# Kernel tuning notes

Measured on AMD Instinct MI355X. Metric: run time of the kernel, lower is better.

## Reference

```python
import jax, jax.numpy as jnp
import numpy as np

VOCAB, S, E, H = 50000, 64, 256, 256
T, B = 512, 64


def _lstm_dir(x_seq, h0, c0, Wih, Whh, bih, bhh):
    """Single-direction LSTM. x_seq: [T,B,E] -> [T,B,H]. PyTorch gate order i,f,g,o."""
    def step(carry, x):
        h, c = carry
        gates = x @ Wih.T + h @ Whh.T + (bih + bhh)  # [B,4H]
        i, f, g, o = jnp.split(gates, 4, axis=-1)
        c = jax.nn.sigmoid(f) * c + jax.nn.sigmoid(i) * jnp.tanh(g)
        h = jax.nn.sigmoid(o) * jnp.tanh(c)
        return (h, c), h
    (_, _), hs = jax.lax.scan(step, (h0, c0), x_seq)
    return hs


def setup_inputs() -> dict:
    key = jax.random.key(0)
    ks = jax.random.split(key, 16)
    k = 1.0 / np.sqrt(H)
    u = lambda kk, shp: jax.random.uniform(kk, shp, jnp.float32, -k, k)
    inp = {
        "obs_seq": jax.random.randint(ks[0], (T, B), 0, VOCAB),
        "h0": jax.random.normal(ks[1], (2, B, H), jnp.float32),
        "c0": jax.random.normal(ks[2], (2, B, H), jnp.float32),
        "embed_table": jax.random.normal(ks[3], (VOCAB, E), jnp.float32),
        "Wih_f": u(ks[4], (4 * H, E)), "Whh_f": u(ks[5], (4 * H, H)),
        "bih_f": u(ks[6], (4 * H,)), "bhh_f": u(ks[7], (4 * H,)),
        "Wih_b": u(ks[8], (4 * H, E)), "Whh_b": u(ks[9], (4 * H, H)),
        "bih_b": u(ks[10], (4 * H,)), "bhh_b": u(ks[11], (4 * H,)),
        "W_lin": u(ks[12], (S, 2 * H)), "b_lin": u(ks[13], (S,)),
        "pairwise": jax.random.normal(ks[14], (S, S), jnp.float32),
        "start": jax.random.normal(jax.random.fold_in(key, 7), (S,), jnp.float32),
        "stop": jax.random.normal(ks[15], (S,), jnp.float32),
    }
    return inp


def reference(obs_seq, h0, c0, embed_table, Wih_f, Whh_f, bih_f, bhh_f,
              Wih_b, Whh_b, bih_b, bhh_b, W_lin, b_lin, pairwise, start, stop):
    # BiLSTM features
    emb = embed_table[obs_seq]  # [T,B,E]
    hs_f = _lstm_dir(emb, h0[0], c0[0], Wih_f, Whh_f, bih_f, bhh_f)
    hs_b = _lstm_dir(emb[::-1], h0[1], c0[1], Wih_b, Whh_b, bih_b, bhh_b)[::-1]
    feats = jnp.concatenate([hs_f, hs_b], axis=-1)  # [T,B,2H]
    # Emission scores
    scores = jnp.einsum('tbf,sf->tbs', feats, W_lin) + b_lin  # [T,B,S]
    # Viterbi DP (max-plus over states)
    delta0 = start[None, :] + scores[0]  # [B,S]

    def vstep(delta, s_t):
        m = delta[:, :, None] + pairwise[None, :, :]  # [B, prev, next]
        bp = jnp.argmax(m, axis=1)                    # [B,S]
        return jnp.max(m, axis=1) + s_t, bp

    delta_T, bps = jax.lax.scan(vstep, delta0, scores[1:])  # bps: [T-1,B,S]
    final = delta_T + stop[None, :]
    max_score = jnp.max(final, axis=-1)          # [B]
    last = jnp.argmax(final, axis=-1)            # [B]

    def bstep(state, bp_t):
        prev = jnp.take_along_axis(bp_t, state[:, None], axis=1)[:, 0]
        return prev, state

    state0, states_rest = jax.lax.scan(bstep, last, bps, reverse=True)
    state_seq = jnp.concatenate([state0[None], states_rest], axis=0)  # [T,B]
    return max_score, state_seq
```

## Files before the change

### kernel.cpp

```cpp
#include <hip/hip_runtime.h>
#include <math.h>

constexpr int TT = 512;
constexpr int BB = 64;
constexpr int EE = 256;
constexpr int HH = 256;
constexpr int SS = 64;
constexpr int BH = BB * HH;
constexpr int SLICE = 2048;
constexpr int DIRSZ = TT * 8 * SLICE;

typedef float v2f __attribute__((ext_vector_type(2)));

__global__ __launch_bounds__(256) void embT_prep(
    const int* __restrict__ obs, const float* __restrict__ embed,
    float* __restrict__ embT2)
{
    const int t   = blockIdx.x;
    const int tid = threadIdx.x;
    const int b   = tid & 63;
    const int kc  = tid >> 6;
    const int tok = obs[t * BB + b];
    const float4* er = (const float4*)(embed + (size_t)tok * EE);
    float* dst = embT2 + ((size_t)t * 8 + (b >> 3)) * SLICE + (b & 7);
    #pragma unroll
    for (int i = 0; i < 16; ++i) {
        const int k4 = kc * 16 + i;
        float4 v = er[k4];
        const int k = k4 * 4;
        dst[(k + 0) * 8] = v.x;
        dst[(k + 1) * 8] = v.y;
        dst[(k + 2) * 8] = v.z;
        dst[(k + 3) * 8] = v.w;
    }
}

__global__ __launch_bounds__(256) void weight_prep(
    const float* __restrict__ Wih_f, const float* __restrict__ Whh_f,
    const float* __restrict__ Wih_b, const float* __restrict__ Whh_b,
    float* __restrict__ WBx, float* __restrict__ WBh)
{
    const int bx  = blockIdx.x;
    const int dir = bx & 1;
    const int ug  = (bx >> 1) & 15;
    const int kc  = bx >> 5;
    const int tid = threadIdx.x;
    const float* Wih = dir ? Wih_b : Wih_f;
    const float* Whh = dir ? Whh_b : Whh_f;
    const size_t base = (((size_t)(dir * 16 + ug) * 8 + kc) * 32) * 64;
    #pragma unroll
    for (int i = 0; i < 8; ++i) {
        const int idx = tid + i * 256;
        const int kl  = idx >> 6;
        const int r   = idx & 63;
        const int row = (r >> 4) * 256 + ug * 16 + (r & 15);
        const int k   = kc * 32 + kl;
        WBx[base + (size_t)kl * 64 + r] = Wih[(size_t)row * EE + k];
        WBh[base + (size_t)kl * 64 + r] = Whh[(size_t)row * HH + k];
    }
}

__global__ __launch_bounds__(512) void lstm_grid(
    const float* __restrict__ embT2,
    const float* __restrict__ WBx, const float* __restrict__ WBh,
    const float* __restrict__ bih_f, const float* __restrict__ bhh_f,
    const float* __restrict__ bih_b, const float* __restrict__ bhh_b,
    const float* __restrict__ h0, const float* __restrict__ c0,
    float* __restrict__ HS2f, float* __restrict__ HS2b)
{
    __shared__ __align__(16) float xbuf[2][SLICE];
    __shared__ __align__(16) float hbuf[SLICE];
    __shared__ float pb[8 * 520];

    const int tid = threadIdx.x;
    const int r   = tid & 63;
    const int kc  = tid >> 6;
    const int bx  = blockIdx.x;
    const int dir = bx & 1;
    const int ug  = (bx >> 1) & 15;
    const int sg  = bx >> 5;
    const int u0  = ug * 16;

    const float* bih = dir ? bih_b : bih_f;
    const float* bhh = dir ? bhh_b : bhh_f;
    float* HS = dir ? HS2b : HS2f;

    const size_t wbase = (((size_t)(dir * 16 + ug) * 8 + kc) * 32) * 64 + r;
    const float* wx = WBx + wbase;
    const float* wh = WBh + wbase;

    const int uL = tid >> 3;
    const int sU = tid & 7;
    float c_reg = 0.0f;
    float bias0 = 0.f, bias1 = 0.f, bias2 = 0.f, bias3 = 0.f;
    if (tid < 128) {
        const int u  = u0 + uL;
        const int bg = sg * 8 + sU;
        c_reg = c0[dir * BH + bg * HH + u];
        bias0 = bih[0 * 256 + u] + bhh[0 * 256 + u];
        bias1 = bih[1 * 256 + u] + bhh[1 * 256 + u];
        bias2 = bih[2 * 256 + u] + bhh[2 * 256 + u];
        bias3 = bih[3 * 256 + u] + bhh[3 * 256 + u];
    }

    {
        const int t0 = dir ? (TT - 1) : 0;
        const float4 xv = *(const float4*)(embT2
            + ((size_t)t0 * 8 + sg) * SLICE + (size_t)tid * 4);
        *(float4*)&xbuf[0][tid * 4] = xv;
        #pragma unroll
        for (int j = 0; j < 4; ++j) {
            const int idx = tid * 4 + j;
            const int u = idx >> 3, s = idx & 7;
            hbuf[idx] = h0[dir * BH + (sg * 8 + s) * HH + u];
        }
    }
    __syncthreads();

    for (int step = 0; step < TT; ++step) {
        const int t   = dir ? (TT - 1 - step) : step;
        const int cur = step & 1;

        v2f A0 = {0.f, 0.f}, A1 = {0.f, 0.f}, A2 = {0.f, 0.f}, A3 = {0.f, 0.f};

        {
            const float4* xb4 = (const float4*)&xbuf[cur][kc * 256];
            #pragma unroll 8
            for (int kl = 0; kl < 32; ++kl) {
                const float wv = wx[kl * 64];
                const v2f w2 = {wv, wv};
                const float4 xa = xb4[kl * 2];
                const float4 xc = xb4[kl * 2 + 1];
                A0 = __builtin_elementwise_fma((v2f){xa.x, xa.y}, w2, A0);
                A1 = __builtin_elementwise_fma((v2f){xa.z, xa.w}, w2, A1);
                A2 = __builtin_elementwise_fma((v2f){xc.x, xc.y}, w2, A2);
                A3 = __builtin_elementwise_fma((v2f){xc.z, xc.w}, w2, A3);
            }
        }

        const bool has_next = (step + 1 < TT);
        float4 xnext;
        if (has_next) {
            const int tn = dir ? (TT - 2 - step) : (step + 1);
            xnext = *(const float4*)(embT2
                + ((size_t)tn * 8 + sg) * SLICE + (size_t)tid * 4);
        }

        if (step > 0) {
            const int tp = dir ? (t + 1) : (t - 1);
            const float* hsrc = HS + ((size_t)tp * 8 + sg) * SLICE
                                + kc * 256 + r;
            float h0v, h1v, h2v, h3v;
            int spins = 0;
            for (;;) {
                asm volatile(
                    "global_load_dword %0, %4, off sc0 sc1\n\t"
                    "global_load_dword %1, %4, off offset:256 sc0 sc1\n\t"
                    "global_load_dword %2, %4, off offset:512 sc0 sc1\n\t"
                    "global_load_dword %3, %4, off offset:768 sc0 sc1\n\t"
                    "s_waitcnt vmcnt(0)"
                    : "=v"(h0v), "=v"(h1v), "=v"(h2v), "=v"(h3v)
                    : "v"(hsrc)
                    : "memory");
                const float ssum = (h0v + h1v) + (h2v + h3v);
                if (!__any(ssum != ssum)) break;
                if (++spins > 200000) break;
            }
            const int hb = kc * 256 + r;
            hbuf[hb      ] = h0v;
            hbuf[hb +  64] = h1v;
            hbuf[hb + 128] = h2v;
            hbuf[hb + 192] = h3v;
        }

        if (has_next) *(float4*)&xbuf[cur ^ 1][tid * 4] = xnext;

        {
            const float4* hb4 = (const float4*)&hbuf[kc * 256];
            #pragma unroll 8
            for (int kl = 0; kl < 32; ++kl) {
                const float wv = wh[kl * 64];
                const v2f w2 = {wv, wv};
                const float4 ha = hb4[kl * 2];
                const float4 hc = hb4[kl * 2 + 1];
                A0 = __builtin_elementwise_fma((v2f){ha.x, ha.y}, w2, A0);
                A1 = __builtin_elementwise_fma((v2f){ha.z, ha.w}, w2, A1);
                A2 = __builtin_elementwise_fma((v2f){hc.x, hc.y}, w2, A2);
                A3 = __builtin_elementwise_fma((v2f){hc.z, hc.w}, w2, A3);
            }
        }

        {
            const int pbi = kc * 64 + r;
            pb[0 * 520 + pbi] = A0.x; pb[1 * 520 + pbi] = A0.y;
            pb[2 * 520 + pbi] = A1.x; pb[3 * 520 + pbi] = A1.y;
            pb[4 * 520 + pbi] = A2.x; pb[5 * 520 + pbi] = A2.y;
            pb[6 * 520 + pbi] = A3.x; pb[7 * 520 + pbi] = A3.y;
        }
        __syncthreads();

        if (tid < 128) {
            float p0 = bias0, p1 = bias1, p2 = bias2, p3 = bias3;
            #pragma unroll
            for (int q = 0; q < 8; ++q) {
                p0 += pb[sU * 520 + q * 64 + 0 * 16 + uL];
                p1 += pb[sU * 520 + q * 64 + 1 * 16 + uL];
                p2 += pb[sU * 520 + q * 64 + 2 * 16 + uL];
                p3 += pb[sU * 520 + q * 64 + 3 * 16 + uL];
            }
            const float ig = 1.0f / (1.0f + expf(-p0));
            const float fg = 1.0f / (1.0f + expf(-p1));
            const float gg = tanhf(p2);
            const float og = 1.0f / (1.0f + expf(-p3));
            c_reg = fg * c_reg + ig * gg;
            const float h = og * tanhf(c_reg);
            unsigned* dst = (unsigned*)(HS + ((size_t)t * 8 + sg) * SLICE
                                        + (u0 + uL) * 8 + sU);
            (void)__hip_atomic_exchange(dst, __float_as_uint(h),
                                        __ATOMIC_RELAXED,
                                        __HIP_MEMORY_SCOPE_AGENT);
        }
    }
}

__global__ __launch_bounds__(256) void scores_kernel(
    const float* __restrict__ HS2f, const float* __restrict__ HS2b,
    const float* __restrict__ W_lin, const float* __restrict__ b_lin,
    float* __restrict__ scores)
{
    __shared__ __align__(16) float As[128 * 64];
    __shared__ __align__(16) float Ws[128 * 64];
    const int t   = blockIdx.x;
    const int tid = threadIdx.x;
    const int bl  = tid & 63;
    const int kc  = tid >> 6;
    const int tb  = tid & 15;
    const int ts  = tid >> 4;

    float acc[4][4] = {};

    for (int chunk = 0; chunk < 4; ++chunk) {
        const int koff = chunk * 128;
        const float* srcH = (koff < 256) ? HS2f : HS2b;
        const int bu = koff & 255;
        #pragma unroll
        for (int i = 0; i < 8; ++i) {
            const int jg = tid + i * 256;
            const int sg = jg >> 8;
            const int j  = jg & 255;
            const int kl = j >> 1;
            const int s0 = (j & 1) * 4;
            const float4 v = *(const float4*)(srcH
                + ((size_t)t * 8 + sg) * SLICE + (size_t)(bu + kl) * 8 + s0);
            *(float4*)&As[kl * 64 + sg * 8 + s0] = v;
        }
        const float4* wl4 = (const float4*)(W_lin + koff);
        #pragma unroll
        for (int it = 0; it < 8; ++it) {
            const int k4 = it * 4 + kc;
            float4 wv = wl4[bl * 128 + k4];
            const int k = k4 * 4;
            Ws[(k + 0) * 64 + bl] = wv.x; Ws[(k + 1) * 64 + bl] = wv.y;
            Ws[(k + 2) * 64 + bl] = wv.z; Ws[(k + 3) * 64 + bl] = wv.w;
        }
        __syncthreads();
        #pragma unroll 4
        for (int k = 0; k < 128; ++k) {
            const float4 av = *(const float4*)&As[k * 64 + tb * 4];
            const float4 bv = *(const float4*)&Ws[k * 64 + ts * 4];
            acc[0][0] += av.x * bv.x; acc[0][1] += av.x * bv.y; acc[0][2] += av.x * bv.z; acc[0][3] += av.x * bv.w;
            acc[1][0] += av.y * bv.x; acc[1][1] += av.y * bv.y; acc[1][2] += av.y * bv.z; acc[1][3] += av.y * bv.w;
            acc[2][0] += av.z * bv.x; acc[2][1] += av.z * bv.y; acc[2][2] += av.z * bv.z; acc[2][3] += av.z * bv.w;
            acc[3][0] += av.w * bv.x; acc[3][1] += av.w * bv.y; acc[3][2] += av.w * bv.z; acc[3][3] += av.w * bv.w;
        }
        __syncthreads();
    }

    #pragma unroll
    for (int i = 0; i < 4; ++i) {
        const int bb = tb * 4 + i;
        #pragma unroll
        for (int j = 0; j < 4; ++j) {
            const int ss = ts * 4 + j;
            scores[(size_t)t * (BB * SS) + bb * SS + ss] = acc[i][j] + b_lin[ss];
        }
    }
}

__global__ __launch_bounds__(256) void viterbi_kernel(
    const float* __restrict__ scores, const float* __restrict__ pairwise,
    const float* __restrict__ start, const float* __restrict__ stop,
    float* __restrict__ out)
{
    __shared__ float delta[2][64];
    __shared__ float part[4][64];
    __shared__ int   pidx[4][64];
    __shared__ unsigned char bps[511 * 64];
    __shared__ float fin[64];

    const int b   = blockIdx.x;
    const int tid = threadIdx.x;
    const int s   = tid & 63;
    const int q   = tid >> 6;

    float pw[16];
    #pragma unroll
    for (int i = 0; i < 16; ++i)
        pw[i] = pairwise[(q * 16 + i) * 64 + s];

    if (q == 0) delta[0][s] = start[s] + scores[b * SS + s];
    __syncthreads();

    int cur = 0;
    for (int t = 1; t < TT; ++t) {
        float sc = 0.0f;
        if (q == 0) sc = scores[(size_t)t * (BB * SS) + b * SS + s];
        float best = -1e30f;
        int bp = q * 16;
        #pragma unroll
        for (int i = 0; i < 16; ++i) {
            const float v = delta[cur][q * 16 + i] + pw[i];
            if (v > best) { best = v; bp = q * 16 + i; }
        }
        part[q][s] = best;
        pidx[q][s] = bp;
        __syncthreads();
        if (q == 0) {
            float m = part[0][s];
            int arg = pidx[0][s];
            #pragma unroll
            for (int qq = 1; qq < 4; ++qq) {
                const float v = part[qq][s];
                if (v > m) { m = v; arg = pidx[qq][s]; }
            }
            delta[cur ^ 1][s] = m + sc;
            bps[(t - 1) * 64 + s] = (unsigned char)arg;
        }
        cur ^= 1;
        __syncthreads();
    }

    if (q == 0) fin[s] = delta[cur][s] + stop[s];
    __syncthreads();

    if (tid == 0) {
        float m = fin[0];
        int arg = 0;
        for (int p = 1; p < 64; ++p)
            if (fin[p] > m) { m = fin[p]; arg = p; }
        out[b] = m;
        int st = arg;
        out[64 + 511 * 64 + b] = (float)st;
        for (int k = 510; k >= 0; --k) {
            st = bps[k * 64 + st];
            out[64 + k * 64 + b] = (float)st;
        }
    }
}

extern "C" void kernel_launch(void* const* d_in, const int* in_sizes, int n_in,
                              void* d_out, int out_size, void* d_ws, size_t ws_size,
                              hipStream_t stream)
{
    const int*   obs      = (const int*)d_in[0];
    const float* h0       = (const float*)d_in[1];
    const float* c0       = (const float*)d_in[2];
    const float* embed    = (const float*)d_in[3];
    const float* Wih_f    = (const float*)d_in[4];
    const float* Whh_f    = (const float*)d_in[5];
    const float* bih_f    = (const float*)d_in[6];
    const float* bhh_f    = (const float*)d_in[7];
    const float* Wih_b    = (const float*)d_in[8];
    const float* Whh_b    = (const float*)d_in[9];
    const float* bih_b    = (const float*)d_in[10];
    const float* bhh_b    = (const float*)d_in[11];
    const float* W_lin    = (const float*)d_in[12];
    const float* b_lin    = (const float*)d_in[13];
    const float* pairwise = (const float*)d_in[14];
    const float* start    = (const float*)d_in[15];
    const float* stop     = (const float*)d_in[16];
    (void)in_sizes; (void)n_in; (void)out_size; (void)ws_size;

    float* ws     = (float*)d_ws;
    float* embT2  = ws;
    float* HS2f   = embT2 + (size_t)DIRSZ;
    float* HS2b   = HS2f + (size_t)DIRSZ;
    float* scores = HS2b + (size_t)DIRSZ;
    float* WBx = scores;
    float* WBh = scores + (size_t)2 * 16 * 8 * 32 * 64;

    hipMemsetAsync(HS2f, 0xFF, (size_t)2 * DIRSZ * sizeof(float), stream);
    embT_prep<<<512, 256, 0, stream>>>(obs, embed, embT2);
    weight_prep<<<256, 256, 0, stream>>>(Wih_f, Whh_f, Wih_b, Whh_b, WBx, WBh);
    lstm_grid<<<256, 512, 0, stream>>>(
        embT2, WBx, WBh, bih_f, bhh_f, bih_b, bhh_b, h0, c0, HS2f, HS2b);
    scores_kernel<<<512, 256, 0, stream>>>(HS2f, HS2b, W_lin, b_lin, scores);
    viterbi_kernel<<<64, 256, 0, stream>>>(scores, pairwise, start, stop, (float*)d_out);
}
```

Before: 2.005 ms.

## Double hidden units per LSTM block, halving persistent grid to 128 blocks

```diff
diff --git a/kernel.cpp b/kernel.cpp
--- a/kernel.cpp
+++ b/kernel.cpp
@@ -42,25 +42,25 @@
 {
     const int bx  = blockIdx.x;
     const int dir = bx & 1;
-    const int ug  = (bx >> 1) & 15;
-    const int kc  = bx >> 5;
+    const int j   = (bx >> 1) & 7;
+    const int kc  = bx >> 4;
     const int tid = threadIdx.x;
     const float* Wih = dir ? Wih_b : Wih_f;
     const float* Whh = dir ? Whh_b : Whh_f;
-    const size_t base = (((size_t)(dir * 16 + ug) * 8 + kc) * 32) * 64;
+    const size_t base = (((size_t)(dir * 8 + j) * 8 + kc) * 32) * 128;
     #pragma unroll
-    for (int i = 0; i < 8; ++i) {
+    for (int i = 0; i < 16; ++i) {
         const int idx = tid + i * 256;
-        const int kl  = idx >> 6;
-        const int r   = idx & 63;
-        const int row = (r >> 4) * 256 + ug * 16 + (r & 15);
+        const int kl  = idx >> 7;
+        const int rg  = idx & 127;
+        const int row = (rg >> 5) * 256 + j * 32 + (rg & 31);
         const int k   = kc * 32 + kl;
-        WBx[base + (size_t)kl * 64 + r] = Wih[(size_t)row * EE + k];
-        WBh[base + (size_t)kl * 64 + r] = Whh[(size_t)row * HH + k];
-    }
-}
-
-__global__ __launch_bounds__(512) void lstm_grid(
+        WBx[base + (size_t)kl * 128 + rg] = Wih[(size_t)row * EE + k];
+        WBh[base + (size_t)kl * 128 + rg] = Whh[(size_t)row * HH + k];
+    }
+}
+
+__global__ __launch_bounds__(1024) void lstm_grid(
     const float* __restrict__ embT2,
     const float* __restrict__ WBx, const float* __restrict__ WBh,
     const float* __restrict__ bih_f, const float* __restrict__ bhh_f,
@@ -69,23 +69,27 @@
     float* __restrict__ HS2f, float* __restrict__ HS2b)
 {
     __shared__ __align__(16) float xbuf[2][SLICE];
-    __shared__ __align__(16) float hbuf[SLICE];
-    __shared__ float pb[8 * 520];
-
-    const int tid = threadIdx.x;
-    const int r   = tid & 63;
-    const int kc  = tid >> 6;
-    const int bx  = blockIdx.x;
-    const int dir = bx & 1;
-    const int ug  = (bx >> 1) & 15;
-    const int sg  = bx >> 5;
-    const int u0  = ug * 16;
+    __shared__ __align__(16) float hbuf[2][SLICE];
+    __shared__ float pb[8 * 1032];
+
+    const int tid  = threadIdx.x;
+    const int r    = tid & 63;
+    const int w    = tid >> 6;
+    const int kc   = w >> 1;
+    const int half = w & 1;
+    const int rg   = half * 64 + r;
+    const int bx   = blockIdx.x;
+    const int g    = bx & 15;
+    const int j    = bx >> 4;
+    const int dir  = g & 1;
+    const int sg   = g >> 1;
+    const int u0   = j * 32;
 
     const float* bih = dir ? bih_b : bih_f;
     const float* bhh = dir ? bhh_b : bhh_f;
     float* HS = dir ? HS2b : HS2f;
 
-    const size_t wbase = (((size_t)(dir * 16 + ug) * 8 + kc) * 32) * 64 + r;
+    const size_t wbase = (((size_t)(dir * 8 + j) * 8 + kc) * 32) * 128 + rg;
     const float* wx = WBx + wbase;
     const float* wh = WBh + wbase;
 
@@ -93,7 +97,7 @@
     const int sU = tid & 7;
     float c_reg = 0.0f;
     float bias0 = 0.f, bias1 = 0.f, bias2 = 0.f, bias3 = 0.f;
-    if (tid < 128) {
+    if (tid < 256) {
         const int u  = u0 + uL;
         const int bg = sg * 8 + sU;
         c_reg = c0[dir * BH + bg * HH + u];
@@ -105,14 +109,16 @@
 
     {
         const int t0 = dir ? (TT - 1) : 0;
-        const float4 xv = *(const float4*)(embT2
-            + ((size_t)t0 * 8 + sg) * SLICE + (size_t)tid * 4);
-        *(float4*)&xbuf[0][tid * 4] = xv;
+        const float2 xv = *(const float2*)(embT2
+            + ((size_t)t0 * 8 + sg) * SLICE + (size_t)tid * 2);
+        *(float2*)&xbuf[0][tid * 2] = xv;
         #pragma unroll
-        for (int j = 0; j < 4; ++j) {
-            const int idx = tid * 4 + j;
+        for (int jj = 0; jj < 2; ++jj) {
+            const int idx = tid * 2 + jj;
             const int u = idx >> 3, s = idx & 7;
-            hbuf[idx] = h0[dir * BH + (sg * 8 + s) * HH + u];
+            const float v = h0[dir * BH + (sg * 8 + s) * HH + u];
+            hbuf[0][idx] = v;
+            hbuf[1][idx] = v;
         }
     }
     __syncthreads();
@@ -127,7 +133,7 @@
             const float4* xb4 = (const float4*)&xbuf[cur][kc * 256];
             #pragma unroll 8
             for (int kl = 0; kl < 32; ++kl) {
-                const float wv = wx[kl * 64];
+                const float wv = wx[kl * 128];
                 const v2f w2 = {wv, wv};
                 const float4 xa = xb4[kl * 2];
                 const float4 xc = xb4[kl * 2 + 1];
@@ -139,11 +145,11 @@
         }
 
         const bool has_next = (step + 1 < TT);
-        float4 xnext;
+        float2 xnext;
         if (has_next) {
             const int tn = dir ? (TT - 2 - step) : (step + 1);
-            xnext = *(const float4*)(embT2
-                + ((size_t)tn * 8 + sg) * SLICE + (size_t)tid * 4);
+            xnext = *(const float2*)(embT2
+                + ((size_t)tn * 8 + sg) * SLICE + (size_t)tid * 2);
         }
 
         if (step > 0) {
@@ -167,19 +173,19 @@
                 if (++spins > 200000) break;
             }
             const int hb = kc * 256 + r;
-            hbuf[hb      ] = h0v;
-            hbuf[hb +  64] = h1v;
-            hbuf[hb + 128] = h2v;
-            hbuf[hb + 192] = h3v;
-        }
-
-        if (has_next) *(float4*)&xbuf[cur ^ 1][tid * 4] = xnext;
+            hbuf[half][hb      ] = h0v;
+            hbuf[half][hb +  64] = h1v;
+            hbuf[half][hb + 128] = h2v;
+            hbuf[half][hb + 192] = h3v;
+        }
+
+        if (has_next) *(float2*)&xbuf[cur ^ 1][tid * 2] = xnext;
 
         {
-            const float4* hb4 = (const float4*)&hbuf[kc * 256];
+            const float4* hb4 = (const float4*)&hbuf[half][kc * 256];
             #pragma unroll 8
             for (int kl = 0; kl < 32; ++kl) {
-                const float wv = wh[kl * 64];
+                const float wv = wh[kl * 128];
                 const v2f w2 = {wv, wv};
                 const float4 ha = hb4[kl * 2];
                 const float4 hc = hb4[kl * 2 + 1];
@@ -191,22 +197,22 @@
         }
 
         {
-            const int pbi = kc * 64 + r;
-            pb[0 * 520 + pbi] = A0.x; pb[1 * 520 + pbi] = A0.y;
-            pb[2 * 520 + pbi] = A1.x; pb[3 * 520 + pbi] = A1.y;
-            pb[4 * 520 + pbi] = A2.x; pb[5 * 520 + pbi] = A2.y;
-            pb[6 * 520 + pbi] = A3.x; pb[7 * 520 + pbi] = A3.y;
+            const int pbi = kc * 128 + rg;
+            pb[0 * 1032 + pbi] = A0.x; pb[1 * 1032 + pbi] = A0.y;
+            pb[2 * 1032 + pbi] = A1.x; pb[3 * 1032 + pbi] = A1.y;
+            pb[4 * 1032 + pbi] = A2.x; pb[5 * 1032 + pbi] = A2.y;
+            pb[6 * 1032 + pbi] = A3.x; pb[7 * 1032 + pbi] = A3.y;
         }
         __syncthreads();
 
-        if (tid < 128) {
+        if (tid < 256) {
             float p0 = bias0, p1 = bias1, p2 = bias2, p3 = bias3;
             #pragma unroll
             for (int q = 0; q < 8; ++q) {
-                p0 += pb[sU * 520 + q * 64 + 0 * 16 + uL];
-                p1 += pb[sU * 520 + q * 64 + 1 * 16 + uL];
-                p2 += pb[sU * 520 + q * 64 + 2 * 16 + uL];
-                p3 += pb[sU * 520 + q * 64 + 3 * 16 + uL];
+                p0 += pb[sU * 1032 + q * 128 + 0 * 32 + uL];
+                p1 += pb[sU * 1032 + q * 128 + 1 * 32 + uL];
+                p2 += pb[sU * 1032 + q * 128 + 2 * 32 + uL];
+                p3 += pb[sU * 1032 + q * 128 + 3 * 32 + uL];
             }
             const float ig = 1.0f / (1.0f + expf(-p0));
             const float fg = 1.0f / (1.0f + expf(-p1));
@@ -387,12 +393,12 @@
     float* HS2b   = HS2f + (size_t)DIRSZ;
     float* scores = HS2b + (size_t)DIRSZ;
     float* WBx = scores;
-    float* WBh = scores + (size_t)2 * 16 * 8 * 32 * 64;
+    float* WBh = scores + (size_t)2 * 8 * 8 * 32 * 128;
 
     hipMemsetAsync(HS2f, 0xFF, (size_t)2 * DIRSZ * sizeof(float), stream);
     embT_prep<<<512, 256, 0, stream>>>(obs, embed, embT2);
-    weight_prep<<<256, 256, 0, stream>>>(Wih_f, Whh_f, Wih_b, Whh_b, WBx, WBh);
-    lstm_grid<<<256, 512, 0, stream>>>(
+    weight_prep<<<128, 256, 0, stream>>>(Wih_f, Whh_f, Wih_b, Whh_b, WBx, WBh);
+    lstm_grid<<<128, 1024, 0, stream>>>(
         embT2, WBx, WBh, bih_f, bhh_f, bih_b, bhh_b, h0, c0, HS2f, HS2b);
     scores_kernel<<<512, 256, 0, stream>>>(HS2f, HS2b, W_lin, b_lin, scores);
     viterbi_kernel<<<64, 256, 0, stream>>>(scores, pairwise, start, stop, (float*)d_out);
```

Measured after the change: 2.831 ms. 1.41x slower.
